# Kernel optimization log

Hardware: AMD Instinct MI355X
Metric: run time of the kernel (lower is better)

## Reference

```python
import jax, jax.numpy as jnp
import numpy as np

N_ATOM = 2048
C_ATOM = 128
C_PAIR = 16
N_HEADS = 4
BLOCK = 128
EPS = 1e-5


def _layernorm(x):
    mu = jnp.mean(x, axis=-1, keepdims=True)
    var = jnp.mean(jnp.square(x - mu), axis=-1, keepdims=True)
    return (x - mu) / jnp.sqrt(var + EPS)


def setup_inputs() -> dict:
    key = jax.random.key(0)
    ks = jax.random.split(key, 12)
    s = 0.02
    x = jax.random.normal(ks[0], (N_ATOM, C_ATOM), jnp.float32)
    pair_emb = jax.random.normal(ks[1], (N_ATOM, N_ATOM, C_PAIR), jnp.float32)
    block_index = jax.random.randint(ks[2], (N_ATOM, BLOCK), 0, N_ATOM, jnp.int64)
    Wq = jax.random.normal(ks[3], (C_ATOM, C_ATOM), jnp.float32) * s
    Wk = jax.random.normal(ks[4], (C_ATOM, C_ATOM), jnp.float32) * s
    Wv = jax.random.normal(ks[5], (C_ATOM, C_ATOM), jnp.float32) * s
    Wb = jax.random.normal(ks[6], (N_HEADS, 1), jnp.float32) * s  # nn.Linear(1, num_heads)
    Wout = jax.random.normal(ks[7], (C_ATOM, C_ATOM), jnp.float32) * s
    W1 = jax.random.normal(ks[8], (4 * C_ATOM, C_ATOM), jnp.float32) * s
    b1 = jnp.zeros((4 * C_ATOM,), jnp.float32)
    W2 = jax.random.normal(ks[9], (C_ATOM, 4 * C_ATOM), jnp.float32) * s
    b2 = jnp.zeros((C_ATOM,), jnp.float32)
    return {"x": x, "pair_emb": pair_emb, "block_index": block_index,
            "Wq": Wq, "Wk": Wk, "Wv": Wv, "Wb": Wb, "Wout": Wout,
            "W1": W1, "b1": b1, "W2": W2, "b2": b2}


def reference(x, pair_emb, block_index, Wq, Wk, Wv, Wb, Wout, W1, b1, W2, b2):
    N = x.shape[0]
    d_head = C_ATOM // N_HEADS
    h = _layernorm(x)
    q = (h @ Wq.T).reshape(N, N_HEADS, d_head)
    k = (h @ Wk.T).reshape(N, N_HEADS, d_head)
    v = (h @ Wv.T).reshape(N, N_HEADS, d_head)

    # pair bias per head: mean over c_pair, then Linear(1 -> n_heads)
    pair_mean = jnp.mean(pair_emb, axis=-1)              # [N, N]
    pair_bias = pair_mean[..., None] * Wb[:, 0]          # [N, N, H]

    # local block-sparse attention: each query i attends to keys block_index[i]
    k_g = k[block_index]                                 # [N, B, H, d]
    v_g = v[block_index]                                 # [N, B, H, d]
    rows = jnp.arange(N)[:, None]
    bias = pair_bias[rows, block_index]                  # [N, B, H]

    scale = 1.0 / jnp.sqrt(jnp.asarray(d_head, q.dtype))
    scores = jnp.einsum('nhd,nbhd->nhb', q, k_g) * scale + jnp.transpose(bias, (0, 2, 1))
    attn = jax.nn.softmax(scores, axis=-1)               # [N, H, B]
    attn_out = jnp.einsum('nhb,nbhd->nhd', attn, v_g).reshape(N, C_ATOM)

    x = x + attn_out @ Wout.T
    h2 = _layernorm(x)
    mlp = jax.nn.silu(h2 @ W1.T + b1) @ W2.T + b2
    return x + mlp
```

## Files before the change

kernel.cpp:

```cpp
#include <hip/hip_runtime.h>
#include <hip/hip_bf16.h>

#define N_ATOMS 2048
#define C_DIM   128
#define C_PAIR  16
#define BLK_K   128
#define LN_EPS  1e-5f

typedef float f32x4 __attribute__((ext_vector_type(4)));
typedef short s16x8 __attribute__((ext_vector_type(8)));

__device__ __forceinline__ float bf_lo(unsigned int p) {
    union { unsigned int i; float f; } u; u.i = p << 16; return u.f;
}
__device__ __forceinline__ float bf_hi(unsigned int p) {
    union { unsigned int i; float f; } u; u.i = p & 0xffff0000u; return u.f;
}
__device__ __forceinline__ unsigned short f2bf(float f) {
    union { float f; unsigned int i; } u; u.f = f;
    const unsigned int r = u.i + 0x7fffu + ((u.i >> 16) & 1u);
    return (unsigned short)(r >> 16);
}

__device__ __forceinline__ s16x8 lda_frag(const unsigned short* base,
                                          int rowBytes, int kstep, int lane) {
    const int m    = lane & 15;
    const int koff = kstep * 64 + ((lane >> 4) << 4);
    const int addr = m * rowBytes + (koff ^ ((m & 7) << 4));
    return *reinterpret_cast<const s16x8*>(
        reinterpret_cast<const char*>(base) + addr);
}

__device__ void pack_unit(int u, int lane,
                          const float* __restrict__ Wout,
                          const float* __restrict__ W1,
                          const float* __restrict__ W2,
                          unsigned short* __restrict__ WoutP,
                          unsigned short* __restrict__ W1P,
                          unsigned short* __restrict__ W2P)
{
    const float* W; unsigned short* P; int K, local;
    if (u < 32)       { W = Wout; P = WoutP; K = 128; local = u; }
    else if (u < 160) { W = W1;   P = W1P;   K = 128; local = u - 32; }
    else              { W = W2;   P = W2P;   K = 512; local = u - 160; }
    const int ksteps = K >> 5;
    const int ntile  = local / ksteps;
    const int kstep  = local - ntile * ksteps;
    const int n  = ntile * 16 + (lane & 15);
    const int k0 = kstep * 32 + ((lane >> 4) << 3);
    const float4* src = reinterpret_cast<const float4*>(W + (size_t)n * K + k0);
    const float4 a = src[0], b = src[1];
    s16x8 o;
    o[0] = (short)f2bf(a.x); o[1] = (short)f2bf(a.y);
    o[2] = (short)f2bf(a.z); o[3] = (short)f2bf(a.w);
    o[4] = (short)f2bf(b.x); o[5] = (short)f2bf(b.y);
    o[6] = (short)f2bf(b.z); o[7] = (short)f2bf(b.w);
    reinterpret_cast<s16x8*>(P)[local * 64 + lane] = o;
}

__global__ __launch_bounds__(512) void ln_qkv_kernel(
    const float* __restrict__ x,
    const float* __restrict__ Wq, const float* __restrict__ Wk,
    const float* __restrict__ Wv,
    const float* __restrict__ Wout, const float* __restrict__ W1,
    const float* __restrict__ W2,
    float* __restrict__ q,
    unsigned short* __restrict__ kb, unsigned short* __restrict__ vb,
    unsigned short* __restrict__ WoutP, unsigned short* __restrict__ W1P,
    unsigned short* __restrict__ W2P)
{
    __shared__ __align__(16) unsigned short hB[16][128];
    const int t = threadIdx.x;
    const int bid = blockIdx.x;
    const int row0 = bid * 16;

    if (t < 64)       pack_unit(bid * 2,     t,       Wout, W1, W2, WoutP, W1P, W2P);
    else if (t < 128) pack_unit(bid * 2 + 1, t - 64,  Wout, W1, W2, WoutP, W1P, W2P);
    else if (t < 192 && bid < 32)
                      pack_unit(256 + bid,   t - 128, Wout, W1, W2, WoutP, W1P, W2P);

    {
        const int r = t >> 5, l = t & 31;
        const float4 xv = reinterpret_cast<const float4*>(
            x + (size_t)(row0 + r) * C_DIM)[l];
        float s  = xv.x + xv.y + xv.z + xv.w;
        float ss = xv.x*xv.x + xv.y*xv.y + xv.z*xv.z + xv.w*xv.w;
        #pragma unroll
        for (int m = 16; m >= 1; m >>= 1) {
            s  += __shfl_xor(s,  m);
            ss += __shfl_xor(ss, m);
        }
        const float mu  = s * (1.0f / 128.0f);
        const float var = ss * (1.0f / 128.0f) - mu * mu;
        const float inv = rsqrtf(var + LN_EPS);
        union { unsigned long long u64; unsigned short u16[4]; } pk;
        pk.u16[0] = f2bf((xv.x - mu) * inv);
        pk.u16[1] = f2bf((xv.y - mu) * inv);
        pk.u16[2] = f2bf((xv.z - mu) * inv);
        pk.u16[3] = f2bf((xv.w - mu) * inv);
        *reinterpret_cast<unsigned long long*>(
            reinterpret_cast<char*>(&hB[0][0]) +
            r * 256 + ((l * 8) ^ ((r & 7) << 4))) = pk.u64;
    }
    __syncthreads();

    {
        const int wv = t >> 6, lane = t & 63;
        s16x8 afr[4];
        #pragma unroll
        for (int ks = 0; ks < 4; ++ks) afr[ks] = lda_frag(&hB[0][0], 256, ks, lane);

        const int n = wv * 16 + (lane & 15);
        #pragma unroll
        for (int p = 0; p < 3; ++p) {
            const float* W = (p == 0) ? Wq : (p == 1) ? Wk : Wv;
            f32x4 acc = {0.f, 0.f, 0.f, 0.f};
            #pragma unroll
            for (int ks = 0; ks < 4; ++ks) {
                const int k0 = ks * 32 + ((lane >> 4) << 3);
                const float4* src = reinterpret_cast<const float4*>(
                    W + (size_t)n * C_DIM + k0);
                const float4 a = src[0], b = src[1];
                s16x8 bfr;
                bfr[0] = (short)f2bf(a.x); bfr[1] = (short)f2bf(a.y);
                bfr[2] = (short)f2bf(a.z); bfr[3] = (short)f2bf(a.w);
                bfr[4] = (short)f2bf(b.x); bfr[5] = (short)f2bf(b.y);
                bfr[6] = (short)f2bf(b.z); bfr[7] = (short)f2bf(b.w);
                acc = __builtin_amdgcn_mfma_f32_16x16x32_bf16(afr[ks], bfr, acc, 0, 0, 0);
            }
            #pragma unroll
            for (int ii = 0; ii < 4; ++ii) {
                const int m = ((lane >> 4) << 2) + ii;
                const size_t off = (size_t)(row0 + m) * C_DIM + n;
                if (p == 0)      q[off]  = acc[ii];
                else if (p == 1) kb[off] = f2bf(acc[ii]);
                else             vb[off] = f2bf(acc[ii]);
            }
        }
    }
}

__global__ __launch_bounds__(512, 4) void attn_mlp_kernel(
    const float* __restrict__ q, const unsigned short* __restrict__ kb,
    const unsigned short* __restrict__ vb, const float* __restrict__ pair,
    const int*  __restrict__ bidx, const float* __restrict__ Wb,
    const float* __restrict__ x,
    const unsigned short* __restrict__ WoutP,
    const unsigned short* __restrict__ W1P, const float* __restrict__ b1,
    const unsigned short* __restrict__ W2P, const float* __restrict__ b2,
    float* __restrict__ out)
{
    __shared__ __align__(16) float qS[8][128];
    __shared__ __align__(16) int   idxS[8][128];
    __shared__ __align__(16) float Sl[8][4][128];
    __shared__ __align__(16) float ys[8][128];
    __shared__ __align__(16) unsigned short aoB[16][128];
    __shared__ __align__(16) unsigned short h2B[16][128];
    __shared__ __align__(16) unsigned short gsB[16][512];

    const int t = threadIdx.x;
    const int row0 = blockIdx.x * 8;
    const int w = t >> 6, lane = t & 63;
    const int row = row0 + w;

    {
        const uint4 z = {0,0,0,0};
        if (t < 128)      reinterpret_cast<uint4*>(&aoB[8][0])[t] = z;
        else if (t < 256) reinterpret_cast<uint4*>(&h2B[8][0])[t - 128] = z;
        reinterpret_cast<uint4*>(&gsB[8][0])[t] = z;
        if (t < 256) {
            const int r2 = t >> 5, l2 = t & 31;
            const float4 xv = reinterpret_cast<const float4*>(
                x + (size_t)(row0 + r2) * C_DIM)[l2];
            *reinterpret_cast<float4*>(&ys[r2][l2 * 4]) = xv;
        }
    }

    const int j0 = bidx[(size_t)row * BLK_K + lane];
    const int j1 = bidx[(size_t)row * BLK_K + 64 + lane];
    idxS[w][lane] = j0;
    idxS[w][64 + lane] = j1;
    {
        const float2 q2 = *reinterpret_cast<const float2*>(
            q + (size_t)row * C_DIM + 2 * lane);
        *reinterpret_cast<float2*>(&qS[w][2 * lane]) = q2;
    }

    const f32x4* pr0 = reinterpret_cast<const f32x4*>(
        pair + ((size_t)row * N_ATOMS + (size_t)j0) * C_PAIR);
    const f32x4* pr1 = reinterpret_cast<const f32x4*>(
        pair + ((size_t)row * N_ATOMS + (size_t)j1) * C_PAIR);
    const f32x4 pa0 = __builtin_nontemporal_load(pr0 + 0);
    const f32x4 pa1 = __builtin_nontemporal_load(pr0 + 1);
    const f32x4 pa2 = __builtin_nontemporal_load(pr0 + 2);
    const f32x4 pa3 = __builtin_nontemporal_load(pr0 + 3);
    const f32x4 pb0 = __builtin_nontemporal_load(pr1 + 0);
    const f32x4 pb1 = __builtin_nontemporal_load(pr1 + 1);
    const f32x4 pb2 = __builtin_nontemporal_load(pr1 + 2);
    const f32x4 pb3 = __builtin_nontemporal_load(pr1 + 3);

    float sc0[4], sc1[4];
    {
        const uint4* kr0 = reinterpret_cast<const uint4*>(kb + (size_t)j0 * C_DIM);
        const uint4* kr1 = reinterpret_cast<const uint4*>(kb + (size_t)j1 * C_DIM);
        #pragma unroll
        for (int h = 0; h < 4; ++h) {
            float a0 = 0.f, a1 = 0.f;
            #pragma unroll
            for (int c = 0; c < 4; ++c) {
                const uint4 k0 = kr0[h * 4 + c];
                const uint4 k1 = kr1[h * 4 + c];
                const float4 qa = *reinterpret_cast<const float4*>(
                    &qS[w][h * 32 + c * 8]);
                const float4 qc = *reinterpret_cast<const float4*>(
                    &qS[w][h * 32 + c * 8 + 4]);
                a0 += bf_lo(k0.x)*qa.x + bf_hi(k0.x)*qa.y
                    + bf_lo(k0.y)*qa.z + bf_hi(k0.y)*qa.w
                    + bf_lo(k0.z)*qc.x + bf_hi(k0.z)*qc.y
                    + bf_lo(k0.w)*qc.z + bf_hi(k0.w)*qc.w;
                a1 += bf_lo(k1.x)*qa.x + bf_hi(k1.x)*qa.y
                    + bf_lo(k1.y)*qa.z + bf_hi(k1.y)*qa.w
                    + bf_lo(k1.z)*qc.x + bf_hi(k1.z)*qc.y
                    + bf_lo(k1.w)*qc.z + bf_hi(k1.w)*qc.w;
            }
            sc0[h] = a0; sc1[h] = a1;
        }
    }

    const float pm0 = (pa0.x+pa0.y+pa0.z+pa0.w + pa1.x+pa1.y+pa1.z+pa1.w +
                       pa2.x+pa2.y+pa2.z+pa2.w + pa3.x+pa3.y+pa3.z+pa3.w) * (1.0f/16.0f);
    const float pm1 = (pb0.x+pb0.y+pb0.z+pb0.w + pb1.x+pb1.y+pb1.z+pb1.w +
                       pb2.x+pb2.y+pb2.z+pb2.w + pb3.x+pb3.y+pb3.z+pb3.w) * (1.0f/16.0f);
    const float scale = 0.17677669529663687f;

    #pragma unroll
    for (int h = 0; h < 4; ++h) {
        const float wb = Wb[h];
        const float s0 = sc0[h] * scale + pm0 * wb;
        const float s1 = sc1[h] * scale + pm1 * wb;
        float mx = fmaxf(s0, s1);
        #pragma unroll
        for (int m = 32; m >= 1; m >>= 1) mx = fmaxf(mx, __shfl_xor(mx, m));
        const float e0 = __expf(s0 - mx), e1 = __expf(s1 - mx);
        float sm = e0 + e1;
        #pragma unroll
        for (int m = 32; m >= 1; m >>= 1) sm += __shfl_xor(sm, m);
        const float rs = 1.0f / sm;
        Sl[w][h][lane]      = e0 * rs;
        Sl[w][h][lane + 64] = e1 * rs;
    }

    {
        const int d0 = 2 * lane;
        const int hh = lane >> 4;
        float acc0 = 0.f, acc1 = 0.f;
        #pragma unroll 8
        for (int k4 = 0; k4 < 32; ++k4) {
            const int4   j4 = *reinterpret_cast<const int4*>(&idxS[w][k4 * 4]);
            const float4 p4 = *reinterpret_cast<const float4*>(&Sl[w][hh][k4 * 4]);
            unsigned int v01;
            v01 = *reinterpret_cast<const unsigned int*>(vb + (size_t)j4.x * C_DIM + d0);
            acc0 += p4.x * bf_lo(v01); acc1 += p4.x * bf_hi(v01);
            v01 = *reinterpret_cast<const unsigned int*>(vb + (size_t)j4.y * C_DIM + d0);
            acc0 += p4.y * bf_lo(v01); acc1 += p4.y * bf_hi(v01);
            v01 = *reinterpret_cast<const unsigned int*>(vb + (size_t)j4.z * C_DIM + d0);
            acc0 += p4.z * bf_lo(v01); acc1 += p4.z * bf_hi(v01);
            v01 = *reinterpret_cast<const unsigned int*>(vb + (size_t)j4.w * C_DIM + d0);
            acc0 += p4.w * bf_lo(v01); acc1 += p4.w * bf_hi(v01);
        }
        const unsigned int pk = (unsigned int)f2bf(acc0) |
                                ((unsigned int)f2bf(acc1) << 16);
        *reinterpret_cast<unsigned int*>(
            reinterpret_cast<char*>(&aoB[0][0]) +
            w * 256 + ((4 * lane) ^ ((w & 7) << 4))) = pk;
    }

    __syncthreads();

    {
        f32x4 acc = {0.f, 0.f, 0.f, 0.f};
        const s16x8* Bp = reinterpret_cast<const s16x8*>(WoutP);
        #pragma unroll
        for (int ks = 0; ks < 4; ++ks) {
            const s16x8 a = lda_frag(&aoB[0][0], 256, ks, lane);
            const s16x8 b = Bp[(w * 4 + ks) * 64 + lane];
            acc = __builtin_amdgcn_mfma_f32_16x16x32_bf16(a, b, acc, 0, 0, 0);
        }
        const int c = w * 16 + (lane & 15);
        #pragma unroll
        for (int i = 0; i < 4; ++i) {
            const int m = ((lane >> 4) << 2) + i;
            if (m < 8) ys[m][c] += acc[i];
        }
    }
    __syncthreads();

    if (t < 256) {
        const int rr = t >> 5, l = t & 31;
        const float4 yv = *reinterpret_cast<const float4*>(&ys[rr][l * 4]);
        float s  = yv.x + yv.y + yv.z + yv.w;
        float ss = yv.x*yv.x + yv.y*yv.y + yv.z*yv.z + yv.w*yv.w;
        #pragma unroll
        for (int m = 16; m >= 1; m >>= 1) {
            s  += __shfl_xor(s,  m);
            ss += __shfl_xor(ss, m);
        }
        const float mu  = s * (1.0f / 128.0f);
        const float var = ss * (1.0f / 128.0f) - mu * mu;
        const float inv = rsqrtf(var + LN_EPS);
        union { unsigned long long u64; unsigned short u16[4]; } pk;
        pk.u16[0] = f2bf((yv.x - mu) * inv);
        pk.u16[1] = f2bf((yv.y - mu) * inv);
        pk.u16[2] = f2bf((yv.z - mu) * inv);
        pk.u16[3] = f2bf((yv.w - mu) * inv);
        *reinterpret_cast<unsigned long long*>(
            reinterpret_cast<char*>(&h2B[0][0]) +
            rr * 256 + ((l * 8) ^ ((rr & 7) << 4))) = pk.u64;
    }
    __syncthreads();

    {
        s16x8 afr[4];
        #pragma unroll
        for (int ks = 0; ks < 4; ++ks) afr[ks] = lda_frag(&h2B[0][0], 256, ks, lane);
        const s16x8* Bp = reinterpret_cast<const s16x8*>(W1P);
        #pragma unroll
        for (int tt = 0; tt < 4; ++tt) {
            const int tile = w * 4 + tt;
            f32x4 acc = {0.f, 0.f, 0.f, 0.f};
            #pragma unroll
            for (int ks = 0; ks < 4; ++ks) {
                const s16x8 b = Bp[(tile * 4 + ks) * 64 + lane];
                acc = __builtin_amdgcn_mfma_f32_16x16x32_bf16(afr[ks], b, acc, 0, 0, 0);
            }
            const int c = tile * 16 + (lane & 15);
            const float bb = b1[c];
            #pragma unroll
            for (int i = 0; i < 4; ++i) {
                const int m = ((lane >> 4) << 2) + i;
                if (m < 8) {
                    const float g = acc[i] + bb;
                    const float sv = g / (1.0f + __expf(-g));
                    *reinterpret_cast<unsigned short*>(
                        reinterpret_cast<char*>(&gsB[0][0]) +
                        m * 1024 + ((c * 2) ^ ((m & 7) << 4))) = f2bf(sv);
                }
            }
        }
    }
    __syncthreads();

    {
        f32x4 acc = {0.f, 0.f, 0.f, 0.f};
        const s16x8* Bp = reinterpret_cast<const s16x8*>(W2P);
        #pragma unroll
        for (int ks = 0; ks < 16; ++ks) {
            const s16x8 a = lda_frag(&gsB[0][0], 1024, ks, lane);
            const s16x8 b = Bp[(w * 16 + ks) * 64 + lane];
            acc = __builtin_amdgcn_mfma_f32_16x16x32_bf16(a, b, acc, 0, 0, 0);
        }
        const int c = w * 16 + (lane & 15);
        const float bb = b2[c];
        #pragma unroll
        for (int i = 0; i < 4; ++i) {
            const int m = ((lane >> 4) << 2) + i;
            if (m < 8)
                out[(size_t)(row0 + m) * C_DIM + c] = ys[m][c] + bb + acc[i];
        }
    }
}

extern "C" void kernel_launch(void* const* d_in, const int* in_sizes, int n_in,
                              void* d_out, int out_size, void* d_ws, size_t ws_size,
                              hipStream_t stream)
{
    const float* x    = (const float*)d_in[0];
    const float* pair = (const float*)d_in[1];
    const int*   bidx = (const int*)  d_in[2];
    const float* Wq   = (const float*)d_in[3];
    const float* Wk   = (const float*)d_in[4];
    const float* Wv   = (const float*)d_in[5];
    const float* Wb   = (const float*)d_in[6];
    const float* Wout = (const float*)d_in[7];
    const float* W1   = (const float*)d_in[8];
    const float* b1   = (const float*)d_in[9];
    const float* W2   = (const float*)d_in[10];
    const float* b2   = (const float*)d_in[11];
    float* out = (float*)d_out;

    char* ws = (char*)d_ws;
    float*          q     = (float*)ws;
    unsigned short* kb    = (unsigned short*)(ws + (1 << 20));
    unsigned short* vb    = (unsigned short*)(ws + (1 << 20) + (1 << 19));
    unsigned short* WoutP = (unsigned short*)(ws + (2 << 20));
    unsigned short* W1P   = (unsigned short*)(ws + (2 << 20) + (32 << 10));
    unsigned short* W2P   = (unsigned short*)(ws + (2 << 20) + (160 << 10));

    hipLaunchKernelGGL(ln_qkv_kernel, dim3(N_ATOMS / 16), dim3(512), 0, stream,
                       x, Wq, Wk, Wv, Wout, W1, W2, q, kb, vb, WoutP, W1P, W2P);
    hipLaunchKernelGGL(attn_mlp_kernel, dim3(N_ATOMS / 8), dim3(512), 0, stream,
                       q, kb, vb, pair, bidx, Wb, x, WoutP, W1P, b1, W2P, b2, out);
}
```

Baseline: 44.88 us.

## Fuse LN/QKV and attention-MLP kernels with a grid-wide atomic barrier

Merges the two kernels into one persistent kernel of 256 blocks of 8 rows each. Each block computes LN and the QKV projection for its own rows, keeps q in shared memory, and issues its pair-embedding loads before the barrier so they overlap the projection. Blocks then wait on a global atomic counter before gathering K/V. This removes a kernel launch and the q round-trip through global memory, but adds a memset launch and a spin barrier that only works if all 256 blocks are resident at once.

```diff
diff --git a/kernel.cpp b/kernel.cpp
--- a/kernel.cpp
+++ b/kernel.cpp
@@ -6,6 +6,7 @@
 #define C_PAIR  16
 #define BLK_K   128
 #define LN_EPS  1e-5f
+#define GRIDB   256
 
 typedef float f32x4 __attribute__((ext_vector_type(4)));
 typedef short s16x8 __attribute__((ext_vector_type(8)));
@@ -58,98 +59,21 @@
     reinterpret_cast<s16x8*>(P)[local * 64 + lane] = o;
 }
 
-__global__ __launch_bounds__(512) void ln_qkv_kernel(
-    const float* __restrict__ x,
+__global__ __launch_bounds__(512, 4) void fused_kernel(
+    const float* __restrict__ x, const float* __restrict__ pair,
+    const int*  __restrict__ bidx,
     const float* __restrict__ Wq, const float* __restrict__ Wk,
-    const float* __restrict__ Wv,
+    const float* __restrict__ Wv, const float* __restrict__ Wb,
     const float* __restrict__ Wout, const float* __restrict__ W1,
-    const float* __restrict__ W2,
-    float* __restrict__ q,
+    const float* __restrict__ b1,  const float* __restrict__ W2,
+    const float* __restrict__ b2,
     unsigned short* __restrict__ kb, unsigned short* __restrict__ vb,
     unsigned short* __restrict__ WoutP, unsigned short* __restrict__ W1P,
-    unsigned short* __restrict__ W2P)
+    unsigned short* __restrict__ W2P,
+    unsigned int* __restrict__ cnt,
+    float* __restrict__ out)
 {
     __shared__ __align__(16) unsigned short hB[16][128];
-    const int t = threadIdx.x;
-    const int bid = blockIdx.x;
-    const int row0 = bid * 16;
-
-    if (t < 64)       pack_unit(bid * 2,     t,       Wout, W1, W2, WoutP, W1P, W2P);
-    else if (t < 128) pack_unit(bid * 2 + 1, t - 64,  Wout, W1, W2, WoutP, W1P, W2P);
-    else if (t < 192 && bid < 32)
-                      pack_unit(256 + bid,   t - 128, Wout, W1, W2, WoutP, W1P, W2P);
-
-    {
-        const int r = t >> 5, l = t & 31;
-        const float4 xv = reinterpret_cast<const float4*>(
-            x + (size_t)(row0 + r) * C_DIM)[l];
-        float s  = xv.x + xv.y + xv.z + xv.w;
-        float ss = xv.x*xv.x + xv.y*xv.y + xv.z*xv.z + xv.w*xv.w;
-        #pragma unroll
-        for (int m = 16; m >= 1; m >>= 1) {
-            s  += __shfl_xor(s,  m);
-            ss += __shfl_xor(ss, m);
-        }
-        const float mu  = s * (1.0f / 128.0f);
-        const float var = ss * (1.0f / 128.0f) - mu * mu;
-        const float inv = rsqrtf(var + LN_EPS);
-        union { unsigned long long u64; unsigned short u16[4]; } pk;
-        pk.u16[0] = f2bf((xv.x - mu) * inv);
-        pk.u16[1] = f2bf((xv.y - mu) * inv);
-        pk.u16[2] = f2bf((xv.z - mu) * inv);
-        pk.u16[3] = f2bf((xv.w - mu) * inv);
-        *reinterpret_cast<unsigned long long*>(
-            reinterpret_cast<char*>(&hB[0][0]) +
-            r * 256 + ((l * 8) ^ ((r & 7) << 4))) = pk.u64;
-    }
-    __syncthreads();
-
-    {
-        const int wv = t >> 6, lane = t & 63;
-        s16x8 afr[4];
-        #pragma unroll
-        for (int ks = 0; ks < 4; ++ks) afr[ks] = lda_frag(&hB[0][0], 256, ks, lane);
-
-        const int n = wv * 16 + (lane & 15);
-        #pragma unroll
-        for (int p = 0; p < 3; ++p) {
-            const float* W = (p == 0) ? Wq : (p == 1) ? Wk : Wv;
-            f32x4 acc = {0.f, 0.f, 0.f, 0.f};
-            #pragma unroll
-            for (int ks = 0; ks < 4; ++ks) {
-                const int k0 = ks * 32 + ((lane >> 4) << 3);
-                const float4* src = reinterpret_cast<const float4*>(
-                    W + (size_t)n * C_DIM + k0);
-                const float4 a = src[0], b = src[1];
-                s16x8 bfr;
-                bfr[0] = (short)f2bf(a.x); bfr[1] = (short)f2bf(a.y);
-                bfr[2] = (short)f2bf(a.z); bfr[3] = (short)f2bf(a.w);
-                bfr[4] = (short)f2bf(b.x); bfr[5] = (short)f2bf(b.y);
-                bfr[6] = (short)f2bf(b.z); bfr[7] = (short)f2bf(b.w);
-                acc = __builtin_amdgcn_mfma_f32_16x16x32_bf16(afr[ks], bfr, acc, 0, 0, 0);
-            }
-            #pragma unroll
-            for (int ii = 0; ii < 4; ++ii) {
-                const int m = ((lane >> 4) << 2) + ii;
-                const size_t off = (size_t)(row0 + m) * C_DIM + n;
-                if (p == 0)      q[off]  = acc[ii];
-                else if (p == 1) kb[off] = f2bf(acc[ii]);
-                else             vb[off] = f2bf(acc[ii]);
-            }
-        }
-    }
-}
-
-__global__ __launch_bounds__(512, 4) void attn_mlp_kernel(
-    const float* __restrict__ q, const unsigned short* __restrict__ kb,
-    const unsigned short* __restrict__ vb, const float* __restrict__ pair,
-    const int*  __restrict__ bidx, const float* __restrict__ Wb,
-    const float* __restrict__ x,
-    const unsigned short* __restrict__ WoutP,
-    const unsigned short* __restrict__ W1P, const float* __restrict__ b1,
-    const unsigned short* __restrict__ W2P, const float* __restrict__ b2,
-    float* __restrict__ out)
-{
     __shared__ __align__(16) float qS[8][128];
     __shared__ __align__(16) int   idxS[8][128];
     __shared__ __align__(16) float Sl[8][4][128];
@@ -159,33 +83,15 @@
     __shared__ __align__(16) unsigned short gsB[16][512];
 
     const int t = threadIdx.x;
-    const int row0 = blockIdx.x * 8;
+    const int bid = blockIdx.x;
     const int w = t >> 6, lane = t & 63;
+    const int row0 = bid * 8;
     const int row = row0 + w;
-
-    {
-        const uint4 z = {0,0,0,0};
-        if (t < 128)      reinterpret_cast<uint4*>(&aoB[8][0])[t] = z;
-        else if (t < 256) reinterpret_cast<uint4*>(&h2B[8][0])[t - 128] = z;
-        reinterpret_cast<uint4*>(&gsB[8][0])[t] = z;
-        if (t < 256) {
-            const int r2 = t >> 5, l2 = t & 31;
-            const float4 xv = reinterpret_cast<const float4*>(
-                x + (size_t)(row0 + r2) * C_DIM)[l2];
-            *reinterpret_cast<float4*>(&ys[r2][l2 * 4]) = xv;
-        }
-    }
 
     const int j0 = bidx[(size_t)row * BLK_K + lane];
     const int j1 = bidx[(size_t)row * BLK_K + 64 + lane];
     idxS[w][lane] = j0;
     idxS[w][64 + lane] = j1;
-    {
-        const float2 q2 = *reinterpret_cast<const float2*>(
-            q + (size_t)row * C_DIM + 2 * lane);
-        *reinterpret_cast<float2*>(&qS[w][2 * lane]) = q2;
-    }
-
     const f32x4* pr0 = reinterpret_cast<const f32x4*>(
         pair + ((size_t)row * N_ATOMS + (size_t)j0) * C_PAIR);
     const f32x4* pr1 = reinterpret_cast<const f32x4*>(
@@ -198,6 +104,95 @@
     const f32x4 pb1 = __builtin_nontemporal_load(pr1 + 1);
     const f32x4 pb2 = __builtin_nontemporal_load(pr1 + 2);
     const f32x4 pb3 = __builtin_nontemporal_load(pr1 + 3);
+
+    if (t < 64)                    pack_unit(bid,       t,      Wout, W1, W2, WoutP, W1P, W2P);
+    else if (bid < 32 && t < 128)  pack_unit(256 + bid, t - 64, Wout, W1, W2, WoutP, W1P, W2P);
+
+    {
+        const uint4 z = {0, 0, 0, 0};
+        reinterpret_cast<uint4*>(&gsB[8][0])[t] = z;
+        if (t < 128)        reinterpret_cast<uint4*>(&aoB[8][0])[t] = z;
+        else if (t < 256)   reinterpret_cast<uint4*>(&h2B[8][0])[t - 128] = z;
+        else if (t < 384)   reinterpret_cast<uint4*>(&hB[8][0])[t - 256] = z;
+    }
+
+    if (t < 256) {
+        const int r = t >> 5, l = t & 31;
+        const float4 xv = reinterpret_cast<const float4*>(
+            x + (size_t)(row0 + r) * C_DIM)[l];
+        *reinterpret_cast<float4*>(&ys[r][l * 4]) = xv;
+        float s  = xv.x + xv.y + xv.z + xv.w;
+        float ss = xv.x*xv.x + xv.y*xv.y + xv.z*xv.z + xv.w*xv.w;
+        #pragma unroll
+        for (int m = 16; m >= 1; m >>= 1) {
+            s  += __shfl_xor(s,  m);
+            ss += __shfl_xor(ss, m);
+        }
+        const float mu  = s * (1.0f / 128.0f);
+        const float var = ss * (1.0f / 128.0f) - mu * mu;
+        const float inv = rsqrtf(var + LN_EPS);
+        union { unsigned long long u64; unsigned short u16[4]; } pk;
+        pk.u16[0] = f2bf((xv.x - mu) * inv);
+        pk.u16[1] = f2bf((xv.y - mu) * inv);
+        pk.u16[2] = f2bf((xv.z - mu) * inv);
+        pk.u16[3] = f2bf((xv.w - mu) * inv);
+        *reinterpret_cast<unsigned long long*>(
+            reinterpret_cast<char*>(&hB[0][0]) +
+            r * 256 + ((l * 8) ^ ((r & 7) << 4))) = pk.u64;
+    }
+    __syncthreads();
+
+    {
+        s16x8 afr[4];
+        #pragma unroll
+        for (int ks = 0; ks < 4; ++ks) afr[ks] = lda_frag(&hB[0][0], 256, ks, lane);
+        const int n = w * 16 + (lane & 15);
+        #pragma unroll
+        for (int p = 0; p < 3; ++p) {
+            const float* W = (p == 0) ? Wq : (p == 1) ? Wk : Wv;
+            f32x4 acc = {0.f, 0.f, 0.f, 0.f};
+            #pragma unroll
+            for (int ks = 0; ks < 4; ++ks) {
+                const int k0 = ks * 32 + ((lane >> 4) << 3);
+                const float4* src = reinterpret_cast<const float4*>(
+                    W + (size_t)n * C_DIM + k0);
+                const float4 a = src[0], b = src[1];
+                s16x8 bfr;
+                bfr[0] = (short)f2bf(a.x); bfr[1] = (short)f2bf(a.y);
+                bfr[2] = (short)f2bf(a.z); bfr[3] = (short)f2bf(a.w);
+                bfr[4] = (short)f2bf(b.x); bfr[5] = (short)f2bf(b.y);
+                bfr[6] = (short)f2bf(b.z); bfr[7] = (short)f2bf(b.w);
+                acc = __builtin_amdgcn_mfma_f32_16x16x32_bf16(afr[ks], bfr, acc, 0, 0, 0);
+            }
+            #pragma unroll
+            for (int ii = 0; ii < 4; ++ii) {
+                const int m = ((lane >> 4) << 2) + ii;
+                if (m < 8) {
+                    const size_t off = (size_t)(row0 + m) * C_DIM + n;
+                    if (p == 0)      qS[m][n] = acc[ii];
+                    else if (p == 1) kb[off] = f2bf(acc[ii]);
+                    else             vb[off] = f2bf(acc[ii]);
+                }
+            }
+        }
+    }
+
+    const float pm0 = (pa0.x+pa0.y+pa0.z+pa0.w + pa1.x+pa1.y+pa1.z+pa1.w +
+                       pa2.x+pa2.y+pa2.z+pa2.w + pa3.x+pa3.y+pa3.z+pa3.w) * (1.0f/16.0f);
+    const float pm1 = (pb0.x+pb0.y+pb0.z+pb0.w + pb1.x+pb1.y+pb1.z+pb1.w +
+                       pb2.x+pb2.y+pb2.z+pb2.w + pb3.x+pb3.y+pb3.z+pb3.w) * (1.0f/16.0f);
+
+    __threadfence();
+    __syncthreads();
+    if (t == 0) {
+        atomicAdd(cnt, 1u);
+        while (__hip_atomic_load(cnt, __ATOMIC_RELAXED,
+                                 __HIP_MEMORY_SCOPE_AGENT) < GRIDB) {
+            __builtin_amdgcn_s_sleep(1);
+        }
+    }
+    __syncthreads();
+    __threadfence();
 
     float sc0[4], sc1[4];
     {
@@ -227,12 +222,7 @@
         }
     }
 
-    const float pm0 = (pa0.x+pa0.y+pa0.z+pa0.w + pa1.x+pa1.y+pa1.z+pa1.w +
-                       pa2.x+pa2.y+pa2.z+pa2.w + pa3.x+pa3.y+pa3.z+pa3.w) * (1.0f/16.0f);
-    const float pm1 = (pb0.x+pb0.y+pb0.z+pb0.w + pb1.x+pb1.y+pb1.z+pb1.w +
-                       pb2.x+pb2.y+pb2.z+pb2.w + pb3.x+pb3.y+pb3.z+pb3.w) * (1.0f/16.0f);
     const float scale = 0.17677669529663687f;
-
     #pragma unroll
     for (int h = 0; h < 4; ++h) {
         const float wb = Wb[h];
@@ -274,7 +264,6 @@
             reinterpret_cast<char*>(&aoB[0][0]) +
             w * 256 + ((4 * lane) ^ ((w & 7) << 4))) = pk;
     }
-
     __syncthreads();
 
     {
@@ -389,15 +378,15 @@
     float* out = (float*)d_out;
 
     char* ws = (char*)d_ws;
-    float*          q     = (float*)ws;
-    unsigned short* kb    = (unsigned short*)(ws + (1 << 20));
-    unsigned short* vb    = (unsigned short*)(ws + (1 << 20) + (1 << 19));
-    unsigned short* WoutP = (unsigned short*)(ws + (2 << 20));
-    unsigned short* W1P   = (unsigned short*)(ws + (2 << 20) + (32 << 10));
-    unsigned short* W2P   = (unsigned short*)(ws + (2 << 20) + (160 << 10));
-
-    hipLaunchKernelGGL(ln_qkv_kernel, dim3(N_ATOMS / 16), dim3(512), 0, stream,
-                       x, Wq, Wk, Wv, Wout, W1, W2, q, kb, vb, WoutP, W1P, W2P);
-    hipLaunchKernelGGL(attn_mlp_kernel, dim3(N_ATOMS / 8), dim3(512), 0, stream,
-                       q, kb, vb, pair, bidx, Wb, x, WoutP, W1P, b1, W2P, b2, out);
-}
+    unsigned short* kb    = (unsigned short*)ws;
+    unsigned short* vb    = (unsigned short*)(ws + (1 << 19));
+    unsigned short* WoutP = (unsigned short*)(ws + (1 << 20));
+    unsigned short* W1P   = (unsigned short*)(ws + (1 << 20) + (32 << 10));
+    unsigned short* W2P   = (unsigned short*)(ws + (1 << 20) + (160 << 10));
+    unsigned int*   cnt   = (unsigned int*)(ws + (2 << 20));
+
+    hipMemsetAsync(cnt, 0, 4, stream);
+    hipLaunchKernelGGL(fused_kernel, dim3(GRIDB), dim3(512), 0, stream,
+                       x, pair, bidx, Wq, Wk, Wv, Wb, Wout, W1, b1, W2, b2,
+                       kb, vb, WoutP, W1P, W2P, cnt, out);
+}
```

Result: slower. 135.9 us (+202.8%).
